# Performance work log

Measured on AMD Instinct MI355X. Metric: run time of the kernel, lower is better.

The kernel has to match this reference:

```python
import jax, jax.numpy as jnp
import numpy as np

C, B, N, IN, OUT = 10, 128, 1152, 8, 16  # num_capsules, batch, num_route_nodes, in_ch, out_ch
NUM_ITERS = 3


def squash(t):
    # t: [..., OUT]
    sq_norm = jnp.sum(t * t, axis=-1, keepdims=True)
    scale = sq_norm / (1.0 + sq_norm)
    return scale * t / jnp.sqrt(sq_norm + 1e-8)


def setup_inputs() -> dict:
    key = jax.random.key(0)
    k1, k2 = jax.random.split(key)
    x = jax.random.normal(k1, (B, N, IN), dtype=jnp.float32)
    route_weights = jax.random.normal(k2, (C, N, IN, OUT), dtype=jnp.float32)
    return {"x": x, "route_weights": route_weights}


def reference(x, route_weights):
    # priors[c,b,n,o] = sum_i x[b,n,i] * W[c,n,i,o]
    priors = jnp.einsum('bni,cnio->cbno', x, route_weights)  # [C,B,N,OUT]
    # torch: logits = zeros_like(priors[:, :, :, 0]) -> [C,B,N,OUT] (dim 3 was the
    # singleton matmul row dim, so the OUT axis survives on the logits)
    logits = jnp.zeros_like(priors)
    outputs = None
    for _ in range(NUM_ITERS):
        attn = jax.nn.softmax(logits, axis=2)            # over route nodes N
        outputs = squash(jnp.sum(attn * priors, axis=2))  # [C,B,OUT]
        # (outputs * priors).sum(-1) broadcasts to [C,B,N,1] added to [C,B,N,OUT]
        logits = logits + jnp.sum(outputs[:, :, None, :] * priors, axis=-1, keepdims=True)
    return outputs  # [C,B,OUT] == outputs.squeeze() in torch (B>1, C>1)
```

## Files before the change

kernel.cpp:

```cpp
#include <hip/hip_runtime.h>


constexpr int C = 10, B = 128, N = 1152, IN = 8, OUT = 16;
constexpr int THREADS = 384;
constexpr int NW = THREADS / 64;
constexpr int G = 2;
constexpr int PASSES = N / (NW * 16);

__global__ __launch_bounds__(THREADS)
void caps_route(const float* __restrict__ Xf, const float* __restrict__ Wf,
                float* __restrict__ Of) {
    __shared__ float lds_s[G][NW][OUT];
    __shared__ float lds_sum[G][NW];
    __shared__ float lds_out[G][OUT];

    const int t = threadIdx.x;
    const int l = t & 63;
    const int wid = t >> 6;
    const int q = l & 3;
    const int rsub = l >> 2;
    const int blk = blockIdx.x;
    const int c = blk >> 6;
    const int b0 = (blk & 63) * G;

    float P[G][PASSES][4];

    #pragma unroll
    for (int p = 0; p < PASSES; ++p) {
        const int n = wid * (16 * PASSES) + p * 16 + rsub;
        const float4* wr = (const float4*)(Wf + (size_t)(c * N + n) * (IN * OUT));
        float4 wv[IN];
        #pragma unroll
        for (int i = 0; i < IN; ++i) wv[i] = wr[i * 4 + q];
        #pragma unroll
        for (int g = 0; g < G; ++g) {
            const float* xb = Xf + ((size_t)((b0 + g) * N + n)) * IN;
            const float4 xa = ((const float4*)xb)[0];
            const float4 xc = ((const float4*)xb)[1];
            const float xs[8] = { xa.x, xa.y, xa.z, xa.w, xc.x, xc.y, xc.z, xc.w };
            float a0 = 0.f, a1 = 0.f, a2 = 0.f, a3 = 0.f;
            #pragma unroll
            for (int i = 0; i < IN; ++i) {
                a0 = fmaf(xs[i], wv[i].x, a0);
                a1 = fmaf(xs[i], wv[i].y, a1);
                a2 = fmaf(xs[i], wv[i].z, a2);
                a3 = fmaf(xs[i], wv[i].w, a3);
            }
            P[g][p][0] = a0; P[g][p][1] = a1; P[g][p][2] = a2; P[g][p][3] = a3;
        }
    }

    float logit[G][PASSES];
    #pragma unroll
    for (int g = 0; g < G; ++g)
        #pragma unroll
        for (int p = 0; p < PASSES; ++p) logit[g][p] = 0.f;

    for (int it = 0; it < 3; ++it) {
        float s4[G][4];
        float ssum[G];
        #pragma unroll
        for (int g = 0; g < G; ++g) {
            ssum[g] = 0.f;
            #pragma unroll
            for (int k = 0; k < 4; ++k) s4[g][k] = 0.f;
        }
        #pragma unroll
        for (int g = 0; g < G; ++g) {
            #pragma unroll
            for (int p = 0; p < PASSES; ++p) {
                const float e = __expf(logit[g][p]);
                ssum[g] += e;
                #pragma unroll
                for (int k = 0; k < 4; ++k) s4[g][k] = fmaf(e, P[g][p][k], s4[g][k]);
            }
        }
        #pragma unroll
        for (int m = 4; m < 64; m <<= 1) {
            #pragma unroll
            for (int g = 0; g < G; ++g) {
                ssum[g] += __shfl_xor(ssum[g], m, 64);
                #pragma unroll
                for (int k = 0; k < 4; ++k) s4[g][k] += __shfl_xor(s4[g][k], m, 64);
            }
        }
        if (l < 4) {
            #pragma unroll
            for (int g = 0; g < G; ++g)
                #pragma unroll
                for (int k = 0; k < 4; ++k) lds_s[g][wid][l * 4 + k] = s4[g][k];
        }
        if (l == 0) {
            #pragma unroll
            for (int g = 0; g < G; ++g) lds_sum[g][wid] = ssum[g];
        }
        __syncthreads();

        if (t < 32) {
            const int g = t >> 4, o = t & 15;
            float so = 0.f, S = 0.f;
            #pragma unroll
            for (int w = 0; w < NW; ++w) { so += lds_s[g][w][o]; S += lds_sum[g][w]; }
            so /= S;
            float r = so * so;
            r += __shfl_xor(r, 1, 64);
            r += __shfl_xor(r, 2, 64);
            r += __shfl_xor(r, 4, 64);
            r += __shfl_xor(r, 8, 64);
            const float ov = so * (r / ((1.f + r) * sqrtf(r + 1e-8f)));
            if (it == 2) Of[((size_t)c * B + b0 + g) * OUT + o] = ov;
            else         lds_out[g][o] = ov;
        }

        if (it < 2) {
            __syncthreads();
            float o4[G][4];
            #pragma unroll
            for (int g = 0; g < G; ++g)
                #pragma unroll
                for (int k = 0; k < 4; ++k) o4[g][k] = lds_out[g][q * 4 + k];
            #pragma unroll
            for (int g = 0; g < G; ++g) {
                #pragma unroll
                for (int p = 0; p < PASSES; ++p) {
                    float d = o4[g][0] * P[g][p][0];
                    d = fmaf(o4[g][1], P[g][p][1], d);
                    d = fmaf(o4[g][2], P[g][p][2], d);
                    d = fmaf(o4[g][3], P[g][p][3], d);
                    d += __shfl_xor(d, 1, 64);
                    d += __shfl_xor(d, 2, 64);
                    logit[g][p] += d;
                }
            }
        }
    }
}

extern "C" void kernel_launch(void* const* d_in, const int* in_sizes, int n_in,
                              void* d_out, int out_size, void* d_ws, size_t ws_size,
                              hipStream_t stream) {
    const float* X = (const float*)d_in[0];
    const float* W = (const float*)d_in[1];
    float* O = (float*)d_out;
    hipLaunchKernelGGL(caps_route, dim3(C * (B / G)), dim3(THREADS), 0, stream, X, W, O);
}
```

Before: 110.6 us.

## Accumulate routing outputs instead of logits and widen blocks to eight waves

Since logits are linear in the outputs, the kernel now keeps a running sum of squashed outputs and recomputes each logit as a dot product of that sum with the priors, rather than storing a logit per prior. The first iteration skips the exponentials entirely because all logits are zero, so it uses plain sums with the normalizer set to the pass count. The block grows from 384 to 512 threads, so each thread holds fewer priors and there are more waves per block. The trade-off is a recomputed dot product plus shuffles inside the softmax loop, and a larger block that may change occupancy.

```diff
diff --git a/kernel.cpp b/kernel.cpp
--- a/kernel.cpp
+++ b/kernel.cpp
@@ -2,7 +2,7 @@
 
 
 constexpr int C = 10, B = 128, N = 1152, IN = 8, OUT = 16;
-constexpr int THREADS = 384;
+constexpr int THREADS = 512;
 constexpr int NW = THREADS / 64;
 constexpr int G = 2;
 constexpr int PASSES = N / (NW * 16);
@@ -34,9 +34,8 @@
         for (int i = 0; i < IN; ++i) wv[i] = wr[i * 4 + q];
         #pragma unroll
         for (int g = 0; g < G; ++g) {
-            const float* xb = Xf + ((size_t)((b0 + g) * N + n)) * IN;
-            const float4 xa = ((const float4*)xb)[0];
-            const float4 xc = ((const float4*)xb)[1];
+            const float4* xr = (const float4*)(Xf + (size_t)((b0 + g) * N + n) * IN);
+            const float4 xa = xr[0], xc = xr[1];
             const float xs[8] = { xa.x, xa.y, xa.z, xa.w, xc.x, xc.y, xc.z, xc.w };
             float a0 = 0.f, a1 = 0.f, a2 = 0.f, a3 = 0.f;
             #pragma unroll
@@ -50,29 +49,46 @@
         }
     }
 
-    float logit[G][PASSES];
+    float oa[G][4];
     #pragma unroll
     for (int g = 0; g < G; ++g)
         #pragma unroll
-        for (int p = 0; p < PASSES; ++p) logit[g][p] = 0.f;
+        for (int k = 0; k < 4; ++k) oa[g][k] = 0.f;
 
     for (int it = 0; it < 3; ++it) {
         float s4[G][4];
         float ssum[G];
-        #pragma unroll
-        for (int g = 0; g < G; ++g) {
-            ssum[g] = 0.f;
+        if (it == 0) {
             #pragma unroll
-            for (int k = 0; k < 4; ++k) s4[g][k] = 0.f;
-        }
-        #pragma unroll
-        for (int g = 0; g < G; ++g) {
+            for (int g = 0; g < G; ++g) {
+                ssum[g] = (float)PASSES;
+                #pragma unroll
+                for (int k = 0; k < 4; ++k) {
+                    float a = 0.f;
+                    #pragma unroll
+                    for (int p = 0; p < PASSES; ++p) a += P[g][p][k];
+                    s4[g][k] = a;
+                }
+            }
+        } else {
             #pragma unroll
-            for (int p = 0; p < PASSES; ++p) {
-                const float e = __expf(logit[g][p]);
-                ssum[g] += e;
+            for (int g = 0; g < G; ++g) {
+                ssum[g] = 0.f;
                 #pragma unroll
-                for (int k = 0; k < 4; ++k) s4[g][k] = fmaf(e, P[g][p][k], s4[g][k]);
+                for (int k = 0; k < 4; ++k) s4[g][k] = 0.f;
+                #pragma unroll
+                for (int p = 0; p < PASSES; ++p) {
+                    float d = oa[g][0] * P[g][p][0];
+                    d = fmaf(oa[g][1], P[g][p][1], d);
+                    d = fmaf(oa[g][2], P[g][p][2], d);
+                    d = fmaf(oa[g][3], P[g][p][3], d);
+                    d += __shfl_xor(d, 1, 64);
+                    d += __shfl_xor(d, 2, 64);
+                    const float e = __expf(d);
+                    ssum[g] += e;
+                    #pragma unroll
+                    for (int k = 0; k < 4; ++k) s4[g][k] = fmaf(e, P[g][p][k], s4[g][k]);
+                }
             }
         }
         #pragma unroll
@@ -114,24 +130,10 @@
 
         if (it < 2) {
             __syncthreads();
-            float o4[G][4];
             #pragma unroll
             for (int g = 0; g < G; ++g)
                 #pragma unroll
-                for (int k = 0; k < 4; ++k) o4[g][k] = lds_out[g][q * 4 + k];
-            #pragma unroll
-            for (int g = 0; g < G; ++g) {
-                #pragma unroll
-                for (int p = 0; p < PASSES; ++p) {
-                    float d = o4[g][0] * P[g][p][0];
-                    d = fmaf(o4[g][1], P[g][p][1], d);
-                    d = fmaf(o4[g][2], P[g][p][2], d);
-                    d = fmaf(o4[g][3], P[g][p][3], d);
-                    d += __shfl_xor(d, 1, 64);
-                    d += __shfl_xor(d, 2, 64);
-                    logit[g][p] += d;
-                }
-            }
+                for (int k = 0; k < 4; ++k) oa[g][k] += lds_out[g][q * 4 + k];
         }
     }
 }
```

New measurement: 99.75 us. 9.8% less time.
